# Kernel tuning notes

Measured on AMD Instinct MI355X. Metric: run time of the kernel, lower is better.

The kernel has to match this reference:

```python
import jax, jax.numpy as jnp
import numpy as np

EMB = 256
D_INNER = 512                         # expand=2 * d_model
HEADDIM = 64
NHEADS = D_INNER // HEADDIM           # 8
DSTATE = 128
DCONV = 4
CONV_DIM = D_INNER + 2 * DSTATE       # 768 (ngroups=1)
D_IN_PROJ = 2 * D_INNER + 2 * DSTATE + NHEADS  # 1288
LN_EPS = 1e-5


def _layernorm(x, w, b):
    m = jnp.mean(x, axis=-1, keepdims=True)
    v = jnp.mean((x - m) ** 2, axis=-1, keepdims=True)
    return (x - m) * jax.lax.rsqrt(v + LN_EPS) * w + b


def _wn_linear(x, g, v, b):
    # torch weight_norm(dim=0): w = g * v / ||v|| per output row
    w = g[:, None] * v / jnp.linalg.norm(v, axis=1, keepdims=True)
    return x @ w.T + b


def _ssm_scan(x, dt, A, Bm, Cm):
    # x: (b,l,h,p)  dt: (b,l,h)  A: (h,)  Bm/Cm: (b,l,n)
    dA = jnp.exp(dt * A)           # (b,l,h), A<0 so dA in (0,1)
    dtx = dt[..., None] * x        # (b,l,h,p)
    bsz = x.shape[0]

    def step(h, inp):
        dA_t, dtx_t, B_t, C_t = inp
        h = h * dA_t[:, :, None, None] + dtx_t[..., None] * B_t[:, None, None, :]
        y = jnp.einsum('bhpn,bn->bhp', h, C_t)
        return h, y

    h0 = jnp.zeros((bsz, NHEADS, HEADDIM, DSTATE), x.dtype)
    xs = (jnp.swapaxes(dA, 0, 1), jnp.swapaxes(dtx, 0, 1),
          jnp.swapaxes(Bm, 0, 1), jnp.swapaxes(Cm, 0, 1))
    _, ys = jax.lax.scan(step, h0, xs)
    return jnp.swapaxes(ys, 0, 1)  # (b,l,h,p)


def _mamba2(u, in_proj_w, conv_w, conv_b, dt_bias, A_log, D_param, ssm_norm_w, out_proj_w):
    B, L, _ = u.shape
    zxbcdt = u @ in_proj_w.T                       # (B,L,1288)
    z_gate = zxbcdt[..., :D_INNER]
    xBC = zxbcdt[..., D_INNER:D_INNER + CONV_DIM]
    dt = zxbcdt[..., D_INNER + CONV_DIM:]
    # causal depthwise conv1d
    xp = jnp.pad(xBC, ((0, 0), (DCONV - 1, 0), (0, 0)))
    xc = jax.lax.conv_general_dilated(
        jnp.swapaxes(xp, 1, 2), conv_w[:, None, :], (1,), 'VALID',
        feature_group_count=CONV_DIM, dimension_numbers=('NCH', 'OIH', 'NCH'))
    xc = jax.nn.silu(jnp.swapaxes(xc, 1, 2) + conv_b)
    x = xc[..., :D_INNER].reshape(B, L, NHEADS, HEADDIM)
    Bm = xc[..., D_INNER:D_INNER + DSTATE]
    Cm = xc[..., D_INNER + DSTATE:]
    dt = jax.nn.softplus(dt + dt_bias)             # (B,L,H)
    A = -jnp.exp(A_log)                            # (H,)
    y = _ssm_scan(x, dt, A, Bm, Cm) + D_param[None, None, :, None] * x
    y = y.reshape(B, L, D_INNER)
    # gated RMSNorm (norm_before_gate=False): rmsnorm(y * silu(z)) * w
    yg = y * jax.nn.silu(z_gate)
    yn = yg * jax.lax.rsqrt(jnp.mean(yg ** 2, axis=-1, keepdims=True) + LN_EPS) * ssm_norm_w
    return yn @ out_proj_w.T


def setup_inputs() -> dict:
    key = jax.random.key(0)
    ks = jax.random.split(key, 12)
    B, NU, NA = 1, 64, 512

    def rn(k, shape, scale):
        return jax.random.normal(k, shape, dtype=jnp.float32) * scale

    z = rn(ks[0], (B, NU, NA, EMB), 1.0)
    in_proj_w = rn(ks[1], (D_IN_PROJ, EMB), EMB ** -0.5)
    conv_w = rn(ks[2], (CONV_DIM, DCONV), DCONV ** -0.5)
    conv_b = rn(ks[3], (CONV_DIM,), 0.02)
    dt_bias = jnp.log(jnp.expm1(jax.random.uniform(ks[4], (NHEADS,), minval=0.001, maxval=0.1)))
    A_log = jnp.log(jax.random.uniform(ks[5], (NHEADS,), minval=1.0, maxval=16.0))
    D_param = jnp.ones((NHEADS,), dtype=jnp.float32)
    ssm_norm_w = jnp.ones((D_INNER,), dtype=jnp.float32)
    out_proj_w = rn(ks[6], (EMB, D_INNER), D_INNER ** -0.5)
    ff_v = rn(ks[7], (EMB, EMB), EMB ** -0.5)
    ff_g = jnp.linalg.norm(ff_v, axis=1)
    ff_b = jnp.zeros((EMB,), dtype=jnp.float32)
    fc1_v = rn(ks[8], (EMB, EMB), EMB ** -0.5)
    fc1_g = jnp.linalg.norm(fc1_v, axis=1)
    fc1_b = jnp.zeros((EMB,), dtype=jnp.float32)
    fc2_v = rn(ks[9], (EMB, EMB), EMB ** -0.5)
    fc2_g = jnp.linalg.norm(fc2_v, axis=1)
    fc2_b = jnp.zeros((EMB,), dtype=jnp.float32)
    return {
        'z': z,
        'ln1_w': jnp.ones((EMB,), dtype=jnp.float32), 'ln1_b': jnp.zeros((EMB,), dtype=jnp.float32),
        'in_proj_w': in_proj_w, 'conv_w': conv_w, 'conv_b': conv_b,
        'dt_bias': dt_bias, 'A_log': A_log, 'D_param': D_param,
        'ssm_norm_w': ssm_norm_w, 'out_proj_w': out_proj_w,
        'ff_g': ff_g, 'ff_v': ff_v, 'ff_b': ff_b,
        'ln2_w': jnp.ones((EMB,), dtype=jnp.float32), 'ln2_b': jnp.zeros((EMB,), dtype=jnp.float32),
        'fc1_g': fc1_g, 'fc1_v': fc1_v, 'fc1_b': fc1_b,
        'fc2_g': fc2_g, 'fc2_v': fc2_v, 'fc2_b': fc2_b,
    }


def reference(z, ln1_w, ln1_b, in_proj_w, conv_w, conv_b, dt_bias, A_log, D_param,
              ssm_norm_w, out_proj_w, ff_g, ff_v, ff_b, ln2_w, ln2_b,
              fc1_g, fc1_v, fc1_b, fc2_g, fc2_v, fc2_b):
    b, nu, na, e = z.shape
    # MambaBlock: z + ff(mamba(norm(z)))
    u = _layernorm(z, ln1_w, ln1_b).reshape(-1, na, e)
    y = _mamba2(u, in_proj_w, conv_w, conv_b, dt_bias, A_log, D_param, ssm_norm_w, out_proj_w)
    y = _wn_linear(y, ff_g, ff_v, ff_b).reshape(b, nu, na, e)
    z = z + y
    # NormFF: z + Lin2(GELU(Lin1(LN(z))))  (dropout inactive in eval)
    h = _layernorm(z, ln2_w, ln2_b)
    h = jax.nn.gelu(_wn_linear(h, fc1_g, fc1_v, fc1_b), approximate=False)
    h = _wn_linear(h, fc2_g, fc2_v, fc2_b)
    return z + h
```

## Files before the change

### kernel.cpp

```cpp
#include <hip/hip_runtime.h>
#include <stdint.h>
#include <math.h>

#define EMB       256
#define D_INNER   512
#define HEADDIM   64
#define NHEADS    8
#define DSTATE    128
#define DCONV     4
#define CONV_DIM  768
#define LN_EPS    1e-5f
#define NBATCH    64
#define SEQLEN    512
#define NTOK      (NBATCH*SEQLEN)

typedef __attribute__((ext_vector_type(8))) short          short8;
typedef __attribute__((ext_vector_type(8))) unsigned short u16x8;
typedef __attribute__((ext_vector_type(4))) float          f32x4;

__device__ __forceinline__ float bfb(unsigned short u) {
    union { unsigned int i; float f; } x; x.i = ((unsigned int)u) << 16; return x.f;
}
__device__ __forceinline__ unsigned short fbf(float f) {
    union { float f; unsigned int i; } x; x.f = f;
    unsigned int i = x.i;
    unsigned int lsb = (i >> 16) & 1u;
    i += 0x7fffu + lsb;
    return (unsigned short)(i >> 16);
}

__global__ __launch_bounds__(256) void cvt_k(const float* __restrict__ in,
                                             unsigned short* __restrict__ out, int n) {
    int i = blockIdx.x * 256 + threadIdx.x;
    if (i < n) out[i] = fbf(in[i]);
}

__global__ __launch_bounds__(256) void ln_k(const float* __restrict__ in,
                                            const float* __restrict__ w,
                                            const float* __restrict__ b,
                                            unsigned short* __restrict__ out) {
    int tok = blockIdx.x, tid = threadIdx.x;
    size_t idx = (size_t)tok * 256 + tid;
    float x = in[idx];
    __shared__ float sm[8];
    float s = x;
    #pragma unroll
    for (int o = 32; o; o >>= 1) s += __shfl_down(s, o);
    if ((tid & 63) == 0) sm[tid >> 6] = s;
    __syncthreads();
    float mean = (sm[0] + sm[1] + sm[2] + sm[3]) * (1.f / 256.f);
    float d = x - mean;
    float q = d * d;
    #pragma unroll
    for (int o = 32; o; o >>= 1) q += __shfl_down(q, o);
    if ((tid & 63) == 0) sm[4 + (tid >> 6)] = q;
    __syncthreads();
    float var = (sm[4] + sm[5] + sm[6] + sm[7]) * (1.f / 256.f);
    out[idx] = fbf(d * rsqrtf(var + LN_EPS) * w[tid] + b[tid]);
}

__global__ __launch_bounds__(256) void wnorm_k(const float* __restrict__ g,
                                               const float* __restrict__ v,
                                               unsigned short* __restrict__ wout) {
    int o = blockIdx.x, tid = threadIdx.x;
    float x = v[(size_t)o * 256 + tid];
    float q = x * x;
    __shared__ float sm[4];
    #pragma unroll
    for (int d = 32; d; d >>= 1) q += __shfl_down(q, d);
    if ((tid & 63) == 0) sm[tid >> 6] = q;
    __syncthreads();
    float tot = sm[0] + sm[1] + sm[2] + sm[3];
    float scale = g[o] * rsqrtf(tot);
    wout[(size_t)o * 256 + tid] = fbf(x * scale);
}

#define BMT 128
#define BNT 128
#define BKT 32
template<int EPI>
__global__ __launch_bounds__(256) void gemm_k(const unsigned short* __restrict__ A,
                                              const unsigned short* __restrict__ Bw,
                                              int K, int N,
                                              unsigned short* __restrict__ out_b,
                                              float* __restrict__ out_f,
                                              const float* __restrict__ bias,
                                              const float* __restrict__ res_f,
                                              unsigned short* __restrict__ out2_b) {
    __shared__ unsigned short As[BMT][BKT + 8];
    __shared__ unsigned short Bs[BNT][BKT + 8];
    int tid = threadIdx.x;
    int bm = blockIdx.x, bn = blockIdx.y;
    int lane = tid & 63, w = tid >> 6;
    int wr = w >> 1, wc = w & 1;
    int fr = lane & 15, fq = lane >> 4;
    f32x4 acc[4][4];
    #pragma unroll
    for (int m = 0; m < 4; m++)
        #pragma unroll
        for (int n = 0; n < 4; n++)
            #pragma unroll
            for (int r = 0; r < 4; r++) acc[m][n][r] = 0.f;

    int r0 = tid >> 2;
    int kc = (tid & 3) << 3;
    for (int k0 = 0; k0 < K; k0 += BKT) {
        __syncthreads();
        *(u16x8*)&As[r0][kc]      = *(const u16x8*)&A[(size_t)(bm * BMT + r0) * K + k0 + kc];
        *(u16x8*)&As[r0 + 64][kc] = *(const u16x8*)&A[(size_t)(bm * BMT + r0 + 64) * K + k0 + kc];
        *(u16x8*)&Bs[r0][kc]      = *(const u16x8*)&Bw[(size_t)(bn * BNT + r0) * K + k0 + kc];
        *(u16x8*)&Bs[r0 + 64][kc] = *(const u16x8*)&Bw[(size_t)(bn * BNT + r0 + 64) * K + k0 + kc];
        __syncthreads();
        short8 af[4], bf_[4];
        #pragma unroll
        for (int m = 0; m < 4; m++) af[m] = *(const short8*)&As[wr * 64 + m * 16 + fr][fq * 8];
        #pragma unroll
        for (int n = 0; n < 4; n++) bf_[n] = *(const short8*)&Bs[wc * 64 + n * 16 + fr][fq * 8];
        #pragma unroll
        for (int m = 0; m < 4; m++)
            #pragma unroll
            for (int n = 0; n < 4; n++)
                acc[m][n] = __builtin_amdgcn_mfma_f32_16x16x32_bf16(af[m], bf_[n], acc[m][n], 0, 0, 0);
    }

    #pragma unroll
    for (int m = 0; m < 4; m++)
        #pragma unroll
        for (int n = 0; n < 4; n++)
            #pragma unroll
            for (int r = 0; r < 4; r++) {
                int grow = bm * BMT + wr * 64 + m * 16 + fq * 4 + r;
                int gcol = bn * BNT + wc * 64 + n * 16 + fr;
                float v = acc[m][n][r];
                if (EPI == 0) {
                    out_b[(size_t)grow * N + gcol] = fbf(v);
                } else if (EPI == 1) {
                    if (gcol < 512) out_b[(size_t)grow * 512 + gcol] = fbf(v);
                    else            out2_b[(size_t)grow * 768 + (gcol - 512)] = fbf(v);
                } else if (EPI == 2) {
                    size_t idx = (size_t)grow * 256 + gcol;
                    out_f[idx] = res_f[idx] + v + bias[gcol];
                } else if (EPI == 3) {
                    size_t idx = (size_t)grow * 256 + gcol;
                    float x = v + bias[gcol];
                    out_b[idx] = fbf(0.5f * x * (1.f + erff(x * 0.70710678118654752f)));
                }
            }
}

__global__ __launch_bounds__(256) void dt_k(const unsigned short* __restrict__ u,
                                            const unsigned short* __restrict__ W,
                                            const float* __restrict__ dtb,
                                            float* __restrict__ dts) {
    int id = blockIdx.x * 256 + threadIdx.x;
    int t = id >> 3, h = id & 7;
    const unsigned short* ur = u + (size_t)t * 256;
    const unsigned short* wr = W + (size_t)(1280 + h) * 256;
    float acc = 0.f;
    for (int k = 0; k < 256; k += 8) {
        u16x8 uv = *(const u16x8*)&ur[k];
        u16x8 wv = *(const u16x8*)&wr[k];
        #pragma unroll
        for (int i = 0; i < 8; i++) acc += bfb(uv[i]) * bfb(wv[i]);
    }
    acc += dtb[h];
    dts[id] = acc > 20.f ? acc : log1pf(expf(acc));
}

__global__ __launch_bounds__(256) void conv_k(unsigned short* xbc,
                                              const float* __restrict__ cw,
                                              const float* __restrict__ cb) {
    int b = blockIdx.y;
    int c0 = blockIdx.x * 64;
    int tid = threadIdx.x;
    int c = tid & 63;
    int rq = tid >> 6;
    __shared__ unsigned short sraw[131][72];
    int ca = c0 + c;
    float w0 = cw[ca * 4 + 0], w1 = cw[ca * 4 + 1];
    float w2 = cw[ca * 4 + 2], w3 = cw[ca * 4 + 3];
    float bias = cb[ca];
    unsigned short carry_u = 0;

    for (int t0 = 0; t0 < 512; t0 += 128) {
        __syncthreads();
        if (tid < 192) sraw[rq][c] = carry_u;
        for (int idx = tid; idx < 1024; idx += 256) {
            int lt = idx >> 3, cg = idx & 7;
            *(u16x8*)&sraw[3 + lt][cg * 8] =
                *(const u16x8*)&xbc[((size_t)(b * 512 + t0 + lt)) * 768 + c0 + cg * 8];
        }
        __syncthreads();
        if (tid < 192) carry_u = sraw[128 + rq][c];
        #pragma unroll 4
        for (int i = 0; i < 32; i++) {
            int lt = rq + 4 * i;
            float acc = bias
                + bfb(sraw[lt + 0][c]) * w0
                + bfb(sraw[lt + 1][c]) * w1
                + bfb(sraw[lt + 2][c]) * w2
                + bfb(sraw[lt + 3][c]) * w3;
            acc = acc / (1.f + expf(-acc));
            xbc[((size_t)(b * 512 + t0 + lt)) * 768 + c0 + c] = fbf(acc);
        }
    }
}

#define CPAD 136
#define TPAD 40
__global__ __launch_bounds__(256) void ssd_k(const unsigned short* __restrict__ xc,
                                             const float* __restrict__ dts,
                                             const float* __restrict__ A_log,
                                             const float* __restrict__ D_param,
                                             unsigned short* __restrict__ y) {
    __shared__ unsigned short Ct[32][CPAD];
    __shared__ unsigned short Bt[32][CPAD];
    __shared__ unsigned short BtT[128][TPAD];
    __shared__ unsigned short XT[64][TPAD];
    __shared__ unsigned short DXT[64][TPAD];
    __shared__ unsigned short DXWT[64][TPAD];
    __shared__ unsigned short LG[32][TPAD];
    __shared__ unsigned short hB[64][CPAD];
    __shared__ unsigned short Yb[32][72];
    __shared__ float scum[32], sdt2[32], sEC[32];
    __shared__ float sET[32][36];

    int bh = blockIdx.x;
    int b = bh >> 3, h = bh & 7;
    int tid = threadIdx.x;
    int w = tid >> 6;
    int lane = tid & 63;
    int fr = lane & 15, fq = lane >> 4;

    float A_h = -expf(A_log[h]);
    float D_h = D_param[h];

    f32x4 hacc[8];
    #pragma unroll
    for (int nf = 0; nf < 8; nf++)
        #pragma unroll
        for (int r = 0; r < 4; r++) hacc[nf][r] = 0.f;

    int t  = tid >> 3;
    int e8 = tid & 7;

    for (int c = 0; c < 16; ++c) {
        size_t tok0 = (size_t)b * 512 + c * 32;
        u16x8 bv0, bv1, cv0, cv1, xv;
        {
            const unsigned short* row = &xc[(tok0 + t) * 768];
            bv0 = *(const u16x8*)&row[512 + e8 * 16];
            bv1 = *(const u16x8*)&row[512 + e8 * 16 + 8];
            cv0 = *(const u16x8*)&row[640 + e8 * 16];
            cv1 = *(const u16x8*)&row[640 + e8 * 16 + 8];
            xv  = *(const u16x8*)&row[h * 64 + e8 * 8];
        }
        *(u16x8*)&Ct[t][e8 * 16]     = cv0;
        *(u16x8*)&Ct[t][e8 * 16 + 8] = cv1;
        *(u16x8*)&Bt[t][e8 * 16]     = bv0;
        *(u16x8*)&Bt[t][e8 * 16 + 8] = bv1;
        #pragma unroll
        for (int j = 0; j < 8; j++) {
            BtT[e8 * 16 + j][t]     = bv0[j];
            BtT[e8 * 16 + 8 + j][t] = bv1[j];
            XT[e8 * 8 + j][t]       = xv[j];
        }
        if (tid < 32) {
            float dtv = dts[(tok0 + tid) * 8 + h];
            sdt2[tid] = dtv;
            float la = dtv * A_h;
            #pragma unroll
            for (int d = 1; d < 32; d <<= 1) {
                float up = __shfl_up(la, d);
                if (lane >= d) la += up;
            }
            scum[tid] = la;
        }
        __syncthreads();
        float cumQ = scum[31];
        if (tid < 32) sEC[tid] = expf(scum[tid]);
        {
            float dtv = sdt2[t];
            float wgt = expf(cumQ - scum[t]);
            #pragma unroll
            for (int j = 0; j < 8; j++) {
                float dtx = dtv * bfb(xv[j]);
                DXT[e8 * 8 + j][t]  = fbf(dtx);
                DXWT[e8 * 8 + j][t] = fbf(wgt * dtx);
            }
        }
        #pragma unroll
        for (int k = 0; k < 4; k++) {
            int idx = tid * 4 + k;
            int tt = idx >> 5, tq = idx & 31;
            sET[tt][tq] = (tq <= tt) ? expf(scum[tt] - scum[tq]) : 0.f;
        }
        #pragma unroll
        for (int nf = 0; nf < 8; nf++)
            #pragma unroll
            for (int r = 0; r < 4; r++)
                hB[w * 16 + fq * 4 + r][nf * 16 + fr] = fbf(hacc[nf][r]);
        __syncthreads();
        if (w == 0) {
            f32x4 g[2][2];
            #pragma unroll
            for (int m = 0; m < 2; m++)
                #pragma unroll
                for (int n = 0; n < 2; n++)
                    #pragma unroll
                    for (int r = 0; r < 4; r++) g[m][n][r] = 0.f;
            #pragma unroll
            for (int ks = 0; ks < 4; ks++) {
                short8 ca0 = *(const short8*)&Ct[fr][ks * 32 + fq * 8];
                short8 ca1 = *(const short8*)&Ct[16 + fr][ks * 32 + fq * 8];
                short8 bb0 = *(const short8*)&Bt[fr][ks * 32 + fq * 8];
                short8 bb1 = *(const short8*)&Bt[16 + fr][ks * 32 + fq * 8];
                g[0][0] = __builtin_amdgcn_mfma_f32_16x16x32_bf16(ca0, bb0, g[0][0], 0, 0, 0);
                g[0][1] = __builtin_amdgcn_mfma_f32_16x16x32_bf16(ca0, bb1, g[0][1], 0, 0, 0);
                g[1][0] = __builtin_amdgcn_mfma_f32_16x16x32_bf16(ca1, bb0, g[1][0], 0, 0, 0);
                g[1][1] = __builtin_amdgcn_mfma_f32_16x16x32_bf16(ca1, bb1, g[1][1], 0, 0, 0);
            }
            #pragma unroll
            for (int m = 0; m < 2; m++)
                #pragma unroll
                for (int nf = 0; nf < 2; nf++)
                    #pragma unroll
                    for (int r = 0; r < 4; r++) {
                        int tt = m * 16 + fq * 4 + r;
                        int tq = nf * 16 + fr;
                        LG[tt][tq] = fbf(g[m][nf][r] * sET[tt][tq]);
                    }
        }
        __syncthreads();
        f32x4 Yi[2];
        #pragma unroll
        for (int m = 0; m < 2; m++)
            #pragma unroll
            for (int r = 0; r < 4; r++) Yi[m][r] = 0.f;
        #pragma unroll
        for (int ks = 0; ks < 4; ks++) {
            short8 a0 = *(const short8*)&Ct[fr][ks * 32 + fq * 8];
            short8 a1 = *(const short8*)&Ct[16 + fr][ks * 32 + fq * 8];
            short8 hb = *(const short8*)&hB[w * 16 + fr][ks * 32 + fq * 8];
            Yi[0] = __builtin_amdgcn_mfma_f32_16x16x32_bf16(a0, hb, Yi[0], 0, 0, 0);
            Yi[1] = __builtin_amdgcn_mfma_f32_16x16x32_bf16(a1, hb, Yi[1], 0, 0, 0);
        }
        #pragma unroll
        for (int m = 0; m < 2; m++)
            #pragma unroll
            for (int r = 0; r < 4; r++) Yi[m][r] *= sEC[m * 16 + fq * 4 + r];
        {
            short8 a0 = *(const short8*)&LG[fr][fq * 8];
            short8 a1 = *(const short8*)&LG[16 + fr][fq * 8];
            short8 dx = *(const short8*)&DXT[w * 16 + fr][fq * 8];
            Yi[0] = __builtin_amdgcn_mfma_f32_16x16x32_bf16(a0, dx, Yi[0], 0, 0, 0);
            Yi[1] = __builtin_amdgcn_mfma_f32_16x16x32_bf16(a1, dx, Yi[1], 0, 0, 0);
        }
        {
            float ecq = sEC[31];
            #pragma unroll
            for (int nf = 0; nf < 8; nf++)
                #pragma unroll
                for (int r = 0; r < 4; r++) hacc[nf][r] *= ecq;
            short8 ax = *(const short8*)&DXWT[w * 16 + fr][fq * 8];
            #pragma unroll
            for (int nf = 0; nf < 8; nf++) {
                short8 bb = *(const short8*)&BtT[nf * 16 + fr][fq * 8];
                hacc[nf] = __builtin_amdgcn_mfma_f32_16x16x32_bf16(ax, bb, hacc[nf], 0, 0, 0);
            }
        }
        #pragma unroll
        for (int m = 0; m < 2; m++)
            #pragma unroll
            for (int r = 0; r < 4; r++) {
                int tt = m * 16 + fq * 4 + r;
                float xf = bfb(XT[w * 16 + fr][tt]);
                Yb[tt][w * 16 + fr] = fbf(Yi[m][r] + D_h * xf);
            }
        __syncthreads();
        {
            u16x8 yv = *(const u16x8*)&Yb[t][e8 * 8];
            *(u16x8*)&y[(tok0 + t) * 512 + h * 64 + e8 * 8] = yv;
        }
    }
}

__global__ __launch_bounds__(256) void gate_k(const unsigned short* __restrict__ y,
                                              const unsigned short* __restrict__ zg,
                                              const float* __restrict__ nw,
                                              unsigned short* __restrict__ yn) {
    int tok = blockIdx.x, tid = threadIdx.x;
    size_t base = (size_t)tok * 512;
    float gv[2];
    float q = 0.f;
    #pragma unroll
    for (int j = 0; j < 2; j++) {
        int c = tid + j * 256;
        float yy = bfb(y[base + c]);
        float zz = bfb(zg[base + c]);
        float s = zz / (1.f + expf(-zz));
        float t = yy * s;
        gv[j] = t;
        q += t * t;
    }
    __shared__ float sm[4];
    #pragma unroll
    for (int o = 32; o; o >>= 1) q += __shfl_down(q, o);
    if ((tid & 63) == 0) sm[tid >> 6] = q;
    __syncthreads();
    float ms = (sm[0] + sm[1] + sm[2] + sm[3]) * (1.f / 512.f);
    float r = rsqrtf(ms + LN_EPS);
    #pragma unroll
    for (int j = 0; j < 2; j++) {
        int c = tid + j * 256;
        yn[base + c] = fbf(gv[j] * r * nw[c]);
    }
}

extern "C" void kernel_launch(void* const* d_in, const int* in_sizes, int n_in,
                              void* d_out, int out_size, void* d_ws, size_t ws_size,
                              hipStream_t stream) {
    if (n_in < 22) return;
    static const int setup_sizes[22] = {8388608,256,256,329728,3072,768,8,8,8,512,
                                        131072,256,65536,256,256,256,256,65536,256,256,65536,256};
    for (int i = 0; i < 22; i++) if (in_sizes[i] != setup_sizes[i]) return;

    const float* z      = (const float*)d_in[0];
    const float* ln1w   = (const float*)d_in[1];
    const float* ln1b   = (const float*)d_in[2];
    const float* inW    = (const float*)d_in[3];
    const float* convw  = (const float*)d_in[4];
    const float* convb  = (const float*)d_in[5];
    const float* dtb    = (const float*)d_in[6];
    const float* Alog   = (const float*)d_in[7];
    const float* Dp     = (const float*)d_in[8];
    const float* normw  = (const float*)d_in[9];
    const float* outW   = (const float*)d_in[10];
    const float* ffg    = (const float*)d_in[11];
    const float* ffv    = (const float*)d_in[12];
    const float* ffb    = (const float*)d_in[13];
    const float* ln2w   = (const float*)d_in[14];
    const float* ln2b   = (const float*)d_in[15];
    const float* fc1g   = (const float*)d_in[16];
    const float* fc1v   = (const float*)d_in[17];
    const float* fc1b   = (const float*)d_in[18];
    const float* fc2g   = (const float*)d_in[19];
    const float* fc2v   = (const float*)d_in[20];
    const float* fc2b   = (const float*)d_in[21];
    float* out = (float*)d_out;
    (void)out_size;

    char* ws = (char*)d_ws;
    const size_t SLOT_A = (size_t)NTOK * 768 * 2;
    const size_t SLOT_B = (size_t)NTOK * 512 * 2;
    const size_t SLOT_C = (size_t)NTOK * 512 * 2;
    const size_t SLOT_D = (size_t)NTOK * 256 * 2;
    const size_t SLOT_E = (size_t)NTOK * 8 * 4;
    const size_t SLOT_W = (size_t)256 * 256 * 2;
    const size_t SLOT_WI = (size_t)1288 * 256 * 2;
    const size_t SLOT_WO = (size_t)256 * 512 * 2;
    char* pA = ws;
    char* pB = pA + SLOT_A;
    char* pC = pB + SLOT_B;
    char* pD = pC + SLOT_C;
    char* pE = pD + SLOT_D;
    char* pW = pE + SLOT_E;
    char* pWI = pW + 3 * SLOT_W;
    char* pWO = pWI + SLOT_WI;
    size_t need = SLOT_A + SLOT_B + SLOT_C + SLOT_D + SLOT_E + 3 * SLOT_W + SLOT_WI + SLOT_WO;
    if (ws_size < need) return;

    unsigned short* xbc = (unsigned short*)pA;
    unsigned short* yn  = (unsigned short*)pA;
    unsigned short* t2  = (unsigned short*)(pA + (size_t)NTOK * 512 * 2);
    unsigned short* y   = (unsigned short*)pB;
    float*          z2  = (float*)pB;
    unsigned short* zgb = (unsigned short*)pC;
    unsigned short* u   = (unsigned short*)pD;
    unsigned short* m1  = (unsigned short*)pD;
    unsigned short* h1  = (unsigned short*)pD;
    float*          dts = (float*)pE;
    unsigned short* wff  = (unsigned short*)pW;
    unsigned short* wfc1 = (unsigned short*)(pW + SLOT_W);
    unsigned short* wfc2 = (unsigned short*)(pW + 2 * SLOT_W);
    unsigned short* inWb = (unsigned short*)pWI;
    unsigned short* outWb = (unsigned short*)pWO;

    cvt_k<<<(1288 * 256 + 255) / 256, 256, 0, stream>>>(inW, inWb, 1288 * 256);
    cvt_k<<<(256 * 512 + 255) / 256, 256, 0, stream>>>(outW, outWb, 256 * 512);
    wnorm_k<<<256, 256, 0, stream>>>(ffg,  ffv,  wff);
    wnorm_k<<<256, 256, 0, stream>>>(fc1g, fc1v, wfc1);
    wnorm_k<<<256, 256, 0, stream>>>(fc2g, fc2v, wfc2);
    ln_k<<<NTOK, 256, 0, stream>>>(z, ln1w, ln1b, u);
    gemm_k<1><<<dim3(256, 10), 256, 0, stream>>>(u, inWb, 256, 1280,
                                                 zgb, nullptr, nullptr, nullptr, xbc);
    dt_k<<<NTOK * 8 / 256, 256, 0, stream>>>(u, inWb, dtb, dts);
    conv_k<<<dim3(12, 64), 256, 0, stream>>>(xbc, convw, convb);
    ssd_k<<<NBATCH * NHEADS, 256, 0, stream>>>(xbc, dts, Alog, Dp, y);
    gate_k<<<NTOK, 256, 0, stream>>>(y, zgb, normw, yn);
    gemm_k<0><<<dim3(256, 2), 256, 0, stream>>>(yn, outWb, 512, 256,
                                                m1, nullptr, nullptr, nullptr, nullptr);
    gemm_k<2><<<dim3(256, 2), 256, 0, stream>>>(m1, wff, 256, 256,
                                                nullptr, z2, ffb, z, nullptr);
    ln_k<<<NTOK, 256, 0, stream>>>(z2, ln2w, ln2b, t2);
    gemm_k<3><<<dim3(256, 2), 256, 0, stream>>>(t2, wfc1, 256, 256,
                                                h1, nullptr, fc1b, nullptr, nullptr);
    gemm_k<2><<<dim3(256, 2), 256, 0, stream>>>(h1, wfc2, 256, 256,
                                                nullptr, out, fc2b, z2, nullptr);
}
```

Baseline: 347.0 us.

## Fuse dt projection into in_proj GEMM, widen K tile, fix SSD LDS conflicts

The separate dt projection kernel is removed. The in_proj GEMM now covers 1288 columns by adding an 11th column tile, and it applies the dt bias and softplus in its epilogue. The GEMM K tile grows from 32 to 64, which halves the number of barrier-separated load iterations at the cost of more LDS. In the SSD kernel, the transposed LDS buffers get extra padding and a row-dependent column offset to reduce bank conflicts. The C·Bᵀ product is also split across all four waves instead of running on one wave. The extra column tile does mostly wasted MFMA work and reads weight rows past 1288.

```diff
diff --git a/kernel.cpp b/kernel.cpp
--- a/kernel.cpp
+++ b/kernel.cpp
@@ -77,7 +77,7 @@
 
 #define BMT 128
 #define BNT 128
-#define BKT 32
+#define BKT 64
 template<int EPI>
 __global__ __launch_bounds__(256) void gemm_k(const unsigned short* __restrict__ A,
                                               const unsigned short* __restrict__ Bw,
@@ -102,25 +102,29 @@
             #pragma unroll
             for (int r = 0; r < 4; r++) acc[m][n][r] = 0.f;
 
-    int r0 = tid >> 2;
-    int kc = (tid & 3) << 3;
+    int r0 = tid >> 3;
+    int kc = (tid & 7) << 3;
     for (int k0 = 0; k0 < K; k0 += BKT) {
         __syncthreads();
-        *(u16x8*)&As[r0][kc]      = *(const u16x8*)&A[(size_t)(bm * BMT + r0) * K + k0 + kc];
-        *(u16x8*)&As[r0 + 64][kc] = *(const u16x8*)&A[(size_t)(bm * BMT + r0 + 64) * K + k0 + kc];
-        *(u16x8*)&Bs[r0][kc]      = *(const u16x8*)&Bw[(size_t)(bn * BNT + r0) * K + k0 + kc];
-        *(u16x8*)&Bs[r0 + 64][kc] = *(const u16x8*)&Bw[(size_t)(bn * BNT + r0 + 64) * K + k0 + kc];
-        __syncthreads();
-        short8 af[4], bf_[4];
-        #pragma unroll
-        for (int m = 0; m < 4; m++) af[m] = *(const short8*)&As[wr * 64 + m * 16 + fr][fq * 8];
-        #pragma unroll
-        for (int n = 0; n < 4; n++) bf_[n] = *(const short8*)&Bs[wc * 64 + n * 16 + fr][fq * 8];
-        #pragma unroll
-        for (int m = 0; m < 4; m++)
-            #pragma unroll
-            for (int n = 0; n < 4; n++)
-                acc[m][n] = __builtin_amdgcn_mfma_f32_16x16x32_bf16(af[m], bf_[n], acc[m][n], 0, 0, 0);
+        #pragma unroll
+        for (int rr = 0; rr < 128; rr += 32) {
+            *(u16x8*)&As[r0 + rr][kc] = *(const u16x8*)&A[(size_t)(bm * BMT + r0 + rr) * K + k0 + kc];
+            *(u16x8*)&Bs[r0 + rr][kc] = *(const u16x8*)&Bw[(size_t)(bn * BNT + r0 + rr) * K + k0 + kc];
+        }
+        __syncthreads();
+        #pragma unroll
+        for (int ks = 0; ks < 2; ks++) {
+            short8 af[4], bf_[4];
+            #pragma unroll
+            for (int m = 0; m < 4; m++) af[m] = *(const short8*)&As[wr * 64 + m * 16 + fr][ks * 32 + fq * 8];
+            #pragma unroll
+            for (int n = 0; n < 4; n++) bf_[n] = *(const short8*)&Bs[wc * 64 + n * 16 + fr][ks * 32 + fq * 8];
+            #pragma unroll
+            for (int m = 0; m < 4; m++)
+                #pragma unroll
+                for (int n = 0; n < 4; n++)
+                    acc[m][n] = __builtin_amdgcn_mfma_f32_16x16x32_bf16(af[m], bf_[n], acc[m][n], 0, 0, 0);
+        }
     }
 
     #pragma unroll
@@ -136,7 +140,12 @@
                     out_b[(size_t)grow * N + gcol] = fbf(v);
                 } else if (EPI == 1) {
                     if (gcol < 512) out_b[(size_t)grow * 512 + gcol] = fbf(v);
-                    else            out2_b[(size_t)grow * 768 + (gcol - 512)] = fbf(v);
+                    else if (gcol < 1280) out2_b[(size_t)grow * 768 + (gcol - 512)] = fbf(v);
+                    else if (gcol < 1288) {
+                        float a2 = v + bias[gcol - 1280];
+                        out_f[(size_t)grow * 8 + (gcol - 1280)] =
+                            a2 > 20.f ? a2 : log1pf(expf(a2));
+                    }
                 } else if (EPI == 2) {
                     size_t idx = (size_t)grow * 256 + gcol;
                     out_f[idx] = res_f[idx] + v + bias[gcol];
@@ -146,25 +155,6 @@
                     out_b[idx] = fbf(0.5f * x * (1.f + erff(x * 0.70710678118654752f)));
                 }
             }
-}
-
-__global__ __launch_bounds__(256) void dt_k(const unsigned short* __restrict__ u,
-                                            const unsigned short* __restrict__ W,
-                                            const float* __restrict__ dtb,
-                                            float* __restrict__ dts) {
-    int id = blockIdx.x * 256 + threadIdx.x;
-    int t = id >> 3, h = id & 7;
-    const unsigned short* ur = u + (size_t)t * 256;
-    const unsigned short* wr = W + (size_t)(1280 + h) * 256;
-    float acc = 0.f;
-    for (int k = 0; k < 256; k += 8) {
-        u16x8 uv = *(const u16x8*)&ur[k];
-        u16x8 wv = *(const u16x8*)&wr[k];
-        #pragma unroll
-        for (int i = 0; i < 8; i++) acc += bfb(uv[i]) * bfb(wv[i]);
-    }
-    acc += dtb[h];
-    dts[id] = acc > 20.f ? acc : log1pf(expf(acc));
 }
 
 __global__ __launch_bounds__(256) void conv_k(unsigned short* xbc,
@@ -207,7 +197,8 @@
 }
 
 #define CPAD 136
-#define TPAD 40
+#define TPAD 48
+#define TOFF(r) ((((r) >> 4) & 1) << 3)
 __global__ __launch_bounds__(256) void ssd_k(const unsigned short* __restrict__ xc,
                                              const float* __restrict__ dts,
                                              const float* __restrict__ A_log,
@@ -219,7 +210,7 @@
     __shared__ unsigned short XT[64][TPAD];
     __shared__ unsigned short DXT[64][TPAD];
     __shared__ unsigned short DXWT[64][TPAD];
-    __shared__ unsigned short LG[32][TPAD];
+    __shared__ unsigned short LG[32][40];
     __shared__ unsigned short hB[64][CPAD];
     __shared__ unsigned short Yb[32][72];
     __shared__ float scum[32], sdt2[32], sEC[32];
@@ -259,11 +250,16 @@
         *(u16x8*)&Ct[t][e8 * 16 + 8] = cv1;
         *(u16x8*)&Bt[t][e8 * 16]     = bv0;
         *(u16x8*)&Bt[t][e8 * 16 + 8] = bv1;
-        #pragma unroll
-        for (int j = 0; j < 8; j++) {
-            BtT[e8 * 16 + j][t]     = bv0[j];
-            BtT[e8 * 16 + 8 + j][t] = bv1[j];
-            XT[e8 * 8 + j][t]       = xv[j];
+        {
+            int tof = TOFF(e8 * 16);
+            #pragma unroll
+            for (int j = 0; j < 8; j++) {
+                BtT[e8 * 16 + j][t + tof]     = bv0[j];
+                BtT[e8 * 16 + 8 + j][t + tof] = bv1[j];
+            }
+            #pragma unroll
+            for (int j = 0; j < 8; j++)
+                XT[e8 * 8 + j][t + TOFF(e8 * 8 + j)] = xv[j];
         }
         if (tid < 32) {
             float dtv = dts[(tok0 + tid) * 8 + h];
@@ -285,8 +281,9 @@
             #pragma unroll
             for (int j = 0; j < 8; j++) {
                 float dtx = dtv * bfb(xv[j]);
-                DXT[e8 * 8 + j][t]  = fbf(dtx);
-                DXWT[e8 * 8 + j][t] = fbf(wgt * dtx);
+                int rr = e8 * 8 + j;
+                DXT[rr][t + TOFF(rr)]  = fbf(dtx);
+                DXWT[rr][t + TOFF(rr)] = fbf(wgt * dtx);
             }
         }
         #pragma unroll
@@ -301,35 +298,23 @@
             for (int r = 0; r < 4; r++)
                 hB[w * 16 + fq * 4 + r][nf * 16 + fr] = fbf(hacc[nf][r]);
         __syncthreads();
-        if (w == 0) {
-            f32x4 g[2][2];
-            #pragma unroll
-            for (int m = 0; m < 2; m++)
-                #pragma unroll
-                for (int n = 0; n < 2; n++)
-                    #pragma unroll
-                    for (int r = 0; r < 4; r++) g[m][n][r] = 0.f;
+        {
+            int m = w >> 1, nf = w & 1;
+            f32x4 g;
+            #pragma unroll
+            for (int r = 0; r < 4; r++) g[r] = 0.f;
             #pragma unroll
             for (int ks = 0; ks < 4; ks++) {
-                short8 ca0 = *(const short8*)&Ct[fr][ks * 32 + fq * 8];
-                short8 ca1 = *(const short8*)&Ct[16 + fr][ks * 32 + fq * 8];
-                short8 bb0 = *(const short8*)&Bt[fr][ks * 32 + fq * 8];
-                short8 bb1 = *(const short8*)&Bt[16 + fr][ks * 32 + fq * 8];
-                g[0][0] = __builtin_amdgcn_mfma_f32_16x16x32_bf16(ca0, bb0, g[0][0], 0, 0, 0);
-                g[0][1] = __builtin_amdgcn_mfma_f32_16x16x32_bf16(ca0, bb1, g[0][1], 0, 0, 0);
-                g[1][0] = __builtin_amdgcn_mfma_f32_16x16x32_bf16(ca1, bb0, g[1][0], 0, 0, 0);
-                g[1][1] = __builtin_amdgcn_mfma_f32_16x16x32_bf16(ca1, bb1, g[1][1], 0, 0, 0);
-            }
-            #pragma unroll
-            for (int m = 0; m < 2; m++)
-                #pragma unroll
-                for (int nf = 0; nf < 2; nf++)
-                    #pragma unroll
-                    for (int r = 0; r < 4; r++) {
-                        int tt = m * 16 + fq * 4 + r;
-                        int tq = nf * 16 + fr;
-                        LG[tt][tq] = fbf(g[m][nf][r] * sET[tt][tq]);
-                    }
+                short8 ca = *(const short8*)&Ct[m * 16 + fr][ks * 32 + fq * 8];
+                short8 bb = *(const short8*)&Bt[nf * 16 + fr][ks * 32 + fq * 8];
+                g = __builtin_amdgcn_mfma_f32_16x16x32_bf16(ca, bb, g, 0, 0, 0);
+            }
+            #pragma unroll
+            for (int r = 0; r < 4; r++) {
+                int tt = m * 16 + fq * 4 + r;
+                int tq = nf * 16 + fr;
+                LG[tt][tq] = fbf(g[r] * sET[tt][tq]);
+            }
         }
         __syncthreads();
         f32x4 Yi[2];
@@ -350,9 +335,10 @@
             #pragma unroll
             for (int r = 0; r < 4; r++) Yi[m][r] *= sEC[m * 16 + fq * 4 + r];
         {
+            int wof = (w & 1) << 3;
             short8 a0 = *(const short8*)&LG[fr][fq * 8];
             short8 a1 = *(const short8*)&LG[16 + fr][fq * 8];
-            short8 dx = *(const short8*)&DXT[w * 16 + fr][fq * 8];
+            short8 dx = *(const short8*)&DXT[w * 16 + fr][fq * 8 + wof];
             Yi[0] = __builtin_amdgcn_mfma_f32_16x16x32_bf16(a0, dx, Yi[0], 0, 0, 0);
             Yi[1] = __builtin_amdgcn_mfma_f32_16x16x32_bf16(a1, dx, Yi[1], 0, 0, 0);
         }
@@ -362,21 +348,25 @@
             for (int nf = 0; nf < 8; nf++)
                 #pragma unroll
                 for (int r = 0; r < 4; r++) hacc[nf][r] *= ecq;
-            short8 ax = *(const short8*)&DXWT[w * 16 + fr][fq * 8];
+            int wof = (w & 1) << 3;
+            short8 ax = *(const short8*)&DXWT[w * 16 + fr][fq * 8 + wof];
             #pragma unroll
             for (int nf = 0; nf < 8; nf++) {
-                short8 bb = *(const short8*)&BtT[nf * 16 + fr][fq * 8];
+                short8 bb = *(const short8*)&BtT[nf * 16 + fr][fq * 8 + ((nf & 1) << 3)];
                 hacc[nf] = __builtin_amdgcn_mfma_f32_16x16x32_bf16(ax, bb, hacc[nf], 0, 0, 0);
             }
         }
-        #pragma unroll
-        for (int m = 0; m < 2; m++)
-            #pragma unroll
-            for (int r = 0; r < 4; r++) {
-                int tt = m * 16 + fq * 4 + r;
-                float xf = bfb(XT[w * 16 + fr][tt]);
-                Yb[tt][w * 16 + fr] = fbf(Yi[m][r] + D_h * xf);
-            }
+        {
+            int wof = (w & 1) << 3;
+            #pragma unroll
+            for (int m = 0; m < 2; m++)
+                #pragma unroll
+                for (int r = 0; r < 4; r++) {
+                    int tt = m * 16 + fq * 4 + r;
+                    float xf = bfb(XT[w * 16 + fr][tt + wof]);
+                    Yb[tt][w * 16 + fr] = fbf(Yi[m][r] + D_h * xf);
+                }
+        }
         __syncthreads();
         {
             u16x8 yv = *(const u16x8*)&Yb[t][e8 * 8];
@@ -492,9 +482,8 @@
     wnorm_k<<<256, 256, 0, stream>>>(fc1g, fc1v, wfc1);
     wnorm_k<<<256, 256, 0, stream>>>(fc2g, fc2v, wfc2);
     ln_k<<<NTOK, 256, 0, stream>>>(z, ln1w, ln1b, u);
-    gemm_k<1><<<dim3(256, 10), 256, 0, stream>>>(u, inWb, 256, 1280,
-                                                 zgb, nullptr, nullptr, nullptr, xbc);
-    dt_k<<<NTOK * 8 / 256, 256, 0, stream>>>(u, inWb, dtb, dts);
+    gemm_k<1><<<dim3(256, 11), 256, 0, stream>>>(u, inWb, 256, 1288,
+                                                 zgb, dts, dtb, nullptr, xbc);
     conv_k<<<dim3(12, 64), 256, 0, stream>>>(xbc, convw, convb);
     ssd_k<<<NBATCH * NHEADS, 256, 0, stream>>>(xbc, dts, Alog, Dp, y);
     gate_k<<<NTOK, 256, 0, stream>>>(y, zgb, normw, yn);
```

Measured after the change: 395.8 us. 1.14x slower.
